# Optimization experiments

Measured on AMD Instinct MI355X. Metric: run time of the kernel, lower is better.

The kernel has to match this reference:

```python
import jax, jax.numpy as jnp
import numpy as np

N = 100000      # nodes
E = 1600000     # edges
H = 32          # hidden_channels
G = 512         # graphs in batch
F_IN = 7        # input node feature dim (fixed by GCNConv(7, H))
RRELU_SLOPE = (1.0 / 8.0 + 1.0 / 3.0) / 2.0  # eval-mode RReLU negative slope


def _rrelu(v):
    return jnp.where(v >= 0, v, RRELU_SLOPE * v)


def _gcn(x, row, col, ew, W, b):
    # GCNConv with normalize=True, add_self_loops=False
    deg = jax.ops.segment_sum(ew, col, num_segments=N)
    dis = jnp.where(deg > 0, jax.lax.rsqrt(deg), 0.0)
    norm = dis[row] * ew * dis[col]            # [E]
    h = x @ W                                  # [N, H]
    out = jax.ops.segment_sum(norm[:, None] * h[row], col, num_segments=N)
    return out + b


def setup_inputs() -> dict:
    key = jax.random.key(0)
    ks = jax.random.split(key, 12)
    s = 0.1
    x = jax.random.normal(ks[0], (N, F_IN), dtype=jnp.float32)
    edge_index = jax.random.randint(ks[1], (2, E), 0, N)
    batch = jnp.sort(jax.random.randint(ks[2], (N,), 0, G))
    edge_weights = jax.random.uniform(ks[3], (E,), dtype=jnp.float32)
    W1 = jax.random.normal(ks[4], (F_IN, H), dtype=jnp.float32) * s
    b1 = jnp.zeros((H,), jnp.float32)
    W2 = jax.random.normal(ks[5], (H, H), dtype=jnp.float32) * s
    b2 = jnp.zeros((H,), jnp.float32)
    Wl1 = jax.random.normal(ks[6], (H, H), dtype=jnp.float32) * s
    bl1 = jnp.zeros((H,), jnp.float32)
    Wl2 = jax.random.normal(ks[7], (H, H), dtype=jnp.float32) * s
    bl2 = jnp.zeros((H,), jnp.float32)
    Wl3 = jax.random.normal(ks[8], (H, 1), dtype=jnp.float32) * s
    bl3 = jnp.zeros((1,), jnp.float32)
    return dict(x=x, edge_index=edge_index, batch=batch, edge_weights=edge_weights,
                W1=W1, b1=b1, W2=W2, b2=b2, Wl1=Wl1, bl1=bl1, Wl2=Wl2, bl2=bl2,
                Wl3=Wl3, bl3=bl3)


def reference(x, edge_index, batch, edge_weights, W1, b1, W2, b2,
              Wl1, bl1, Wl2, bl2, Wl3, bl3):
    row, col = edge_index[0], edge_index[1]
    # conv1 (weighted GCN)
    x = _gcn(x, row, col, edge_weights, W1, b1)
    # max_pool_neighbor_x: max over incoming neighbors + self-loop
    self_idx = jnp.arange(N)
    x = jax.ops.segment_max(
        jnp.concatenate([x[row], x], axis=0),
        jnp.concatenate([col, self_idx], axis=0),
        num_segments=N)
    res = x
    # conv2 (unit edge weights)
    ones_ew = jnp.ones((E,), x.dtype)
    x = _gcn(x, row, col, ones_ew, W2, b2)
    x = jax.nn.relu(res + x)
    # global max pool over graphs
    x = jax.ops.segment_max(x, batch, num_segments=G)   # [G, H]
    res = x
    x = x @ Wl1 + bl1
    x = _rrelu(res + x)
    res = x
    x = x @ Wl2 + bl2
    x = _rrelu(res + x)
    # dropout: identity in eval mode
    x = x @ Wl3 + bl3
    return _rrelu(x)                                     # [G, 1]
```

## Files before the change

### kernel.cpp

```cpp
#include <hip/hip_runtime.h>
#include <hip/hip_bf16.h>

#define NN 100000
#define EE 1600000
#define HH 32
#define GG 512
#define FIN 7
#define NBUK 391
#define EPB 4096
#define P1G 391
#define BCAP 4608
#define SLOPE 0.22916666666666666f
#define QS 32767.0f
#define IQS (1.0f / 32767.0f)
#define RMASK 0x1FFFFu

typedef unsigned short bf16_t;
typedef unsigned int uint32;
typedef unsigned long long uint64;
typedef unsigned short u16v2 __attribute__((ext_vector_type(2)));

__device__ __forceinline__ bf16_t f2b(float f) {
    return (bf16_t)(__bfloat16_as_ushort(__float2bfloat16(f)));
}
__device__ __forceinline__ float b2f(bf16_t u) {
    return __uint_as_float(((uint32)u) << 16);
}
__device__ __forceinline__ float lo16(uint32 u) { return __uint_as_float(u << 16); }
__device__ __forceinline__ float hi16(uint32 u) { return __uint_as_float(u & 0xFFFF0000u); }
__device__ __forceinline__ uint32 pack2(float a, float b) {
    return (uint32)f2b(a) | ((uint32)f2b(b) << 16);
}
__device__ __forceinline__ uint32 fwd16(uint32 u) {
    return u ^ (0x80008000u | (((u >> 15) & 0x00010001u) * 0x7FFFu));
}
__device__ __forceinline__ uint32 inv16(uint32 w) {
    return w ^ (0x80008000u | ((((~w) >> 15) & 0x00010001u) * 0x7FFFu));
}
__device__ __forceinline__ uint32 pkmax(uint32 a, uint32 b) {
    u16v2 x = __builtin_bit_cast(u16v2, a);
    u16v2 y = __builtin_bit_cast(u16v2, b);
    u16v2 r = __builtin_elementwise_max(x, y);
    return __builtin_bit_cast(uint32, r);
}

__global__ __launch_bounds__(512) void k_p1(const int* __restrict__ row,
                                            const int* __restrict__ col,
                                            const float* __restrict__ ew,
                                            int* __restrict__ Pmat,
                                            uint64* __restrict__ pay) {
    __shared__ int h[512];
    __shared__ int cur[392];
    __shared__ int colc[EPB];
    int t = threadIdx.x;
    h[t] = 0;
    __syncthreads();
    int e0 = blockIdx.x * EPB, e1 = min(e0 + EPB, EE);
    int nloc = e1 - e0;
    for (int i = t; i < nloc; i += 512) {
        int c = col[e0 + i];
        colc[i] = c;
        atomicAdd(&h[c >> 8], 1);
    }
    __syncthreads();
    int c0 = h[t];
    for (int d = 1; d < 512; d <<= 1) {
        int a = (t >= d) ? h[t - d] : 0;
        __syncthreads();
        h[t] += a;
        __syncthreads();
    }
    int ex0 = h[t] - c0;
    if (t < 392) { cur[t] = ex0; Pmat[blockIdx.x * 392 + t] = ex0; }
    __syncthreads();
    uint64* bpay = pay + (size_t)blockIdx.x * EPB;
    for (int i = t; i < nloc; i += 512) {
        int c = colc[i];
        int e = e0 + i;
        uint32 q = (uint32)(ew[e] * QS + 0.5f);
        int r = atomicAdd(&cur[c >> 8], 1);
        bpay[r] = ((uint64)(uint32)(c & 255) << 32) | ((uint64)q << 17) | (uint32)row[e];
    }
}

__global__ __launch_bounds__(256) void k_p2(const int* __restrict__ Pmat,
                                            const uint64* __restrict__ pay,
                                            const float* __restrict__ x,
                                            uint32* __restrict__ spack,
                                            int* __restrict__ cnt,
                                            int* __restrict__ off,
                                            float* __restrict__ d1s,
                                            float* __restrict__ d2,
                                            uint32* __restrict__ xsu) {
    __shared__ uint64 staged[BCAP];
    __shared__ int hist[256], s[256], cur[256], qsum[256];
    __shared__ int tot;
    int b = blockIdx.x, t = threadIdx.x;
    hist[t] = 0; qsum[t] = 0;
    if (t == 0) tot = 0;
    __syncthreads();
    for (int k = t; k < P1G; k += 256) {
        int s0 = Pmat[k * 392 + b];
        int s1 = Pmat[k * 392 + b + 1];
        int len = s1 - s0;
        if (len > 0) {
            int r0 = atomicAdd(&tot, len);
            const uint64* src = pay + (size_t)k * EPB + s0;
            for (int i = 0; i < len && r0 + i < BCAP; i++) staged[r0 + i] = src[i];
        }
    }
    __syncthreads();
    int M = min(tot, BCAP);
    for (int j = t; j < M; j += 256) atomicAdd(&hist[(int)(staged[j] >> 32)], 1);
    __syncthreads();
    int v = hist[t]; s[t] = v;
    __syncthreads();
    for (int d = 1; d < 256; d <<= 1) {
        int u = (t >= d) ? s[t - d] : 0;
        __syncthreads();
        s[t] += u;
        __syncthreads();
    }
    int excl = s[t] - v;
    int gb = b * BCAP;
    int n = b * 256 + t;
    if (n < NN) { cnt[n] = v; off[n] = gb + excl; }
    cur[t] = excl;
    __syncthreads();
    for (int j = t; j < M; j += 256) {
        uint64 p = staged[j];
        int nb = (int)(p >> 32);
        int r = atomicAdd(&cur[nb], 1);
        spack[gb + r] = (uint32)p;
        atomicAdd(&qsum[nb], (int)((uint32)p >> 17));
    }
    __syncthreads();
    if (n < NN) {
        int sq = qsum[t];
        float dis1 = sq > 0 ? rsqrtf((float)sq * IQS) : 0.0f;
        d1s[n] = dis1 * IQS;
        d2[n] = v > 0 ? rsqrtf((float)v) : 0.0f;
        float f0 = x[n * FIN + 0] * dis1, f1 = x[n * FIN + 1] * dis1;
        float f2 = x[n * FIN + 2] * dis1, f3 = x[n * FIN + 3] * dis1;
        float f4 = x[n * FIN + 4] * dis1, f5 = x[n * FIN + 5] * dis1;
        float f6 = x[n * FIN + 6] * dis1;
        xsu[n * 4 + 0] = pack2(f0, f1);
        xsu[n * 4 + 1] = pack2(f2, f3);
        xsu[n * 4 + 2] = pack2(f4, f5);
        xsu[n * 4 + 3] = pack2(f6, 0.0f);
    }
}

__global__ __launch_bounds__(256) void k_agg1(const int* __restrict__ off,
                                              const int* __restrict__ cnt,
                                              const uint32* __restrict__ spack,
                                              const uint4* __restrict__ XS,
                                              const float* __restrict__ d1s,
                                              const float* __restrict__ b1,
                                              const float* __restrict__ W1,
                                              uint32* __restrict__ x1u) {
    __shared__ float sW[FIN * HH];
    int t = threadIdx.x;
    if (t < FIN * HH) sW[t] = W1[t];
    __syncthreads();
    int n = blockIdx.x * 16 + (t >> 4);
    int l = t & 15;
    int o = off[n], m = cnt[n];
    const uint32* bin = spack + o;
    float a0 = 0, a1 = 0, a2 = 0, a3 = 0, a4 = 0, a5 = 0, a6 = 0;
    for (int j = l; j < m; j += 16) {
        uint32 p = bin[j];
        uint4 v = XS[p & RMASK];
        float q = (float)(p >> 17);
        a0 += q * lo16(v.x); a1 += q * hi16(v.x);
        a2 += q * lo16(v.y); a3 += q * hi16(v.y);
        a4 += q * lo16(v.z); a5 += q * hi16(v.z);
        a6 += q * lo16(v.w);
    }
#pragma unroll
    for (int q = 8; q >= 1; q >>= 1) {
        a0 += __shfl_xor(a0, q, 16); a1 += __shfl_xor(a1, q, 16);
        a2 += __shfl_xor(a2, q, 16); a3 += __shfl_xor(a3, q, 16);
        a4 += __shfl_xor(a4, q, 16); a5 += __shfl_xor(a5, q, 16);
        a6 += __shfl_xor(a6, q, 16);
    }
    float sc = d1s[n];
    int c0 = 2 * l, c1 = 2 * l + 1;
    float s0 = a0 * sW[c0] + a1 * sW[HH + c0] + a2 * sW[2 * HH + c0]
             + a3 * sW[3 * HH + c0] + a4 * sW[4 * HH + c0]
             + a5 * sW[5 * HH + c0] + a6 * sW[6 * HH + c0];
    float s1 = a0 * sW[c1] + a1 * sW[HH + c1] + a2 * sW[2 * HH + c1]
             + a3 * sW[3 * HH + c1] + a4 * sW[4 * HH + c1]
             + a5 * sW[5 * HH + c1] + a6 * sW[6 * HH + c1];
    x1u[n * 16 + l] = fwd16(pack2(sc * s0 + b1[c0], sc * s1 + b1[c1]));
}

__global__ __launch_bounds__(256) void k_pool(const int* __restrict__ off,
                                              const int* __restrict__ cnt,
                                              const uint32* __restrict__ spack,
                                              const uint32* __restrict__ X1,
                                              const float* __restrict__ d2,
                                              uint32* __restrict__ xpu,
                                              uint32* __restrict__ xpsu) {
    int t = threadIdx.x;
    int n = blockIdx.x * 4 + (t >> 6);
    int l = t & 63;
    int eg = l >> 2, qt = l & 3;
    int o = off[n], m = cnt[n];
    const uint32* bin = spack + o;
    const uint4* X4 = (const uint4*)X1;
    uint32 binw = (l < m) ? bin[l] : 0;
    uint4 u = X4[n * 4 + qt];
    uint32 t0 = u.x, t1 = u.y, t2 = u.z, t3 = u.w;
    int mc = min(m, 64);
    for (int j0 = 0; j0 < mc; j0 += 16) {
        int j = j0 + eg;
        uint32 p = (uint32)__shfl((int)binw, j, 64);
        int r = (j < mc) ? (int)(p & RMASK) : n;
        uint4 v = X4[r * 4 + qt];
        t0 = pkmax(t0, v.x); t1 = pkmax(t1, v.y);
        t2 = pkmax(t2, v.z); t3 = pkmax(t3, v.w);
    }
    for (int j0 = 64; j0 < m; j0 += 16) {
        int j = j0 + eg;
        int r = (j < m) ? (int)(bin[j] & RMASK) : n;
        uint4 v = X4[r * 4 + qt];
        t0 = pkmax(t0, v.x); t1 = pkmax(t1, v.y);
        t2 = pkmax(t2, v.z); t3 = pkmax(t3, v.w);
    }
#pragma unroll
    for (int o2 = 4; o2 < 64; o2 <<= 1) {
        t0 = pkmax(t0, (uint32)__shfl_xor((int)t0, o2, 64));
        t1 = pkmax(t1, (uint32)__shfl_xor((int)t1, o2, 64));
        t2 = pkmax(t2, (uint32)__shfl_xor((int)t2, o2, 64));
        t3 = pkmax(t3, (uint32)__shfl_xor((int)t3, o2, 64));
    }
    if (eg == 0) {
        uint32 r0 = inv16(t0), r1 = inv16(t1), r2 = inv16(t2), r3 = inv16(t3);
        float dn = d2[n];
        uint4 w0, w1;
        w0.x = r0; w0.y = r1; w0.z = r2; w0.w = r3;
        w1.x = pack2(dn * lo16(r0), dn * hi16(r0));
        w1.y = pack2(dn * lo16(r1), dn * hi16(r1));
        w1.z = pack2(dn * lo16(r2), dn * hi16(r2));
        w1.w = pack2(dn * lo16(r3), dn * hi16(r3));
        ((uint4*)xpu)[n * 4 + qt] = w0;
        ((uint4*)xpsu)[n * 4 + qt] = w1;
    }
}

__global__ __launch_bounds__(256) void k_agg2(const int* __restrict__ off,
                                              const int* __restrict__ cnt,
                                              const uint32* __restrict__ spack,
                                              const uint32* __restrict__ XPS,
                                              float* __restrict__ Sf) {
    int t = threadIdx.x;
    int n = blockIdx.x * 4 + (t >> 6);
    int l = t & 63;
    int eg = l >> 2, qt = l & 3;
    int o = off[n], m = cnt[n];
    const uint32* bin = spack + o;
    const uint4* X4 = (const uint4*)XPS;
    uint32 binw = (l < m) ? bin[l] : 0;
    float a0 = 0, a1 = 0, a2 = 0, a3 = 0, a4 = 0, a5 = 0, a6 = 0, a7 = 0;
    int mc = min(m, 64);
    for (int j0 = 0; j0 < mc; j0 += 16) {
        int j = j0 + eg;
        uint32 p = (uint32)__shfl((int)binw, j, 64);
        if (j < mc) {
            uint4 v = X4[(p & RMASK) * 4 + qt];
            a0 += lo16(v.x); a1 += hi16(v.x);
            a2 += lo16(v.y); a3 += hi16(v.y);
            a4 += lo16(v.z); a5 += hi16(v.z);
            a6 += lo16(v.w); a7 += hi16(v.w);
        }
    }
    for (int j0 = 64; j0 < m; j0 += 16) {
        int j = j0 + eg;
        if (j < m) {
            uint4 v = X4[(bin[j] & RMASK) * 4 + qt];
            a0 += lo16(v.x); a1 += hi16(v.x);
            a2 += lo16(v.y); a3 += hi16(v.y);
            a4 += lo16(v.z); a5 += hi16(v.z);
            a6 += lo16(v.w); a7 += hi16(v.w);
        }
    }
#pragma unroll
    for (int o2 = 4; o2 < 64; o2 <<= 1) {
        a0 += __shfl_xor(a0, o2, 64); a1 += __shfl_xor(a1, o2, 64);
        a2 += __shfl_xor(a2, o2, 64); a3 += __shfl_xor(a3, o2, 64);
        a4 += __shfl_xor(a4, o2, 64); a5 += __shfl_xor(a5, o2, 64);
        a6 += __shfl_xor(a6, o2, 64); a7 += __shfl_xor(a7, o2, 64);
    }
    if (eg == 0) {
        float4 f0 = make_float4(a0, a1, a2, a3);
        float4 f1 = make_float4(a4, a5, a6, a7);
        ((float4*)Sf)[n * 8 + qt * 2] = f0;
        ((float4*)Sf)[n * 8 + qt * 2 + 1] = f1;
    }
}

__global__ __launch_bounds__(256) void k_gpool_mlp(const float* __restrict__ Sf,
                                                   const uint32* __restrict__ xpu,
                                                   const float* __restrict__ d2,
                                                   const float* __restrict__ b2,
                                                   const float* __restrict__ W2,
                                                   const int* __restrict__ batch,
                                                   const float* __restrict__ Wl1,
                                                   const float* __restrict__ bl1,
                                                   const float* __restrict__ Wl2,
                                                   const float* __restrict__ bl2,
                                                   const float* __restrict__ Wl3,
                                                   const float* __restrict__ bl3,
                                                   float* __restrict__ out) {
    __shared__ float sWc[HH * HH];
    __shared__ float sW1[HH * HH];
    __shared__ float sW2[HH * HH];
    __shared__ float sW3[HH];
    __shared__ float sred[8][HH];
    int t = threadIdx.x;
    int g = blockIdx.x;
    for (int j = t; j < HH * HH; j += 256) {
        sWc[j] = W2[j];
        sW1[j] = Wl1[j];
        sW2[j] = Wl2[j];
    }
    if (t < HH) sW3[t] = Wl3[t];
    __syncthreads();

    int lo = 0, hi = NN;
    while (lo < hi) { int mid = (lo + hi) >> 1; if (batch[mid] < g) lo = mid + 1; else hi = mid; }
    int s = lo;
    hi = NN;
    while (lo < hi) { int mid = (lo + hi) >> 1; if (batch[mid] < g + 1) lo = mid + 1; else hi = mid; }
    int e = lo;

    int c = t & 31, w = t >> 5;
    float bc = b2[c];
    float mx = -3.0e38f;
    for (int i = s + w; i < e; i += 8) {
        float sv = Sf[i * HH + c];
        float acc = 0.0f;
#pragma unroll
        for (int k = 0; k < HH; k++) acc += __shfl(sv, k, 32) * sWc[k * HH + c];
        uint32 u = xpu[i * 16 + (c >> 1)];
        float xpv = (c & 1) ? hi16(u) : lo16(u);
        float v = fmaxf(xpv + d2[i] * acc + bc, 0.0f);
        v = b2f(f2b(v));
        mx = fmaxf(mx, v);
    }
    sred[w][c] = mx;
    __syncthreads();

    if (t < HH) {
        float x0 = sred[0][t];
#pragma unroll
        for (int q = 1; q < 8; q++) x0 = fmaxf(x0, sred[q][t]);
        float acc = 0.0f;
#pragma unroll
        for (int k = 0; k < HH; k++) acc += __shfl(x0, k, 32) * sW1[k * HH + t];
        float a1 = x0 + acc + bl1[t];
        a1 = a1 >= 0.0f ? a1 : SLOPE * a1;
        float acc2 = 0.0f;
#pragma unroll
        for (int k = 0; k < HH; k++) acc2 += __shfl(a1, k, 32) * sW2[k * HH + t];
        float a2 = a1 + acc2 + bl2[t];
        a2 = a2 >= 0.0f ? a2 : SLOPE * a2;
        float p = a2 * sW3[t];
#pragma unroll
        for (int o = 16; o >= 1; o >>= 1) p += __shfl_down(p, o, 32);
        if (t == 0) {
            float o = p + bl3[0];
            o = o >= 0.0f ? o : SLOPE * o;
            out[g] = o;
        }
    }
}

extern "C" void kernel_launch(void* const* d_in, const int* in_sizes, int n_in,
                              void* d_out, int out_size, void* d_ws, size_t ws_size,
                              hipStream_t stream) {
    const float* x   = (const float*)d_in[0];
    const int*   ei  = (const int*)d_in[1];
    const int*   bat = (const int*)d_in[2];
    const float* ew  = (const float*)d_in[3];
    const float* W1  = (const float*)d_in[4];
    const float* b1  = (const float*)d_in[5];
    const float* W2  = (const float*)d_in[6];
    const float* b2  = (const float*)d_in[7];
    const float* Wl1 = (const float*)d_in[8];
    const float* bl1 = (const float*)d_in[9];
    const float* Wl2 = (const float*)d_in[10];
    const float* bl2 = (const float*)d_in[11];
    const float* Wl3 = (const float*)d_in[12];
    const float* bl3 = (const float*)d_in[13];
    float* out = (float*)d_out;

    const int* row = ei;
    const int* col = ei + EE;

    char* w = (char*)d_ws;
    uint64* pay  = (uint64*)w;  w += (size_t)P1G * EPB * 8;
    float*  Sf   = (float*)pay;
    int*   Pmat  = (int*)w;     w += (size_t)P1G * 392 * 4;
    uint32* spack = (uint32*)w; w += (size_t)NBUK * BCAP * 4;
    int*    cnt  = (int*)w;     w += NN * 4;
    int*    off  = (int*)w;     w += NN * 4;
    float*  d1s  = (float*)w;   w += NN * 4;
    float*  d2   = (float*)w;   w += NN * 4;
    uint32* xsu  = (uint32*)w;  w += (size_t)NN * 4 * 4;
    uint32* x1u  = (uint32*)w;  w += (size_t)NN * 16 * 4;
    uint32* xpu  = (uint32*)w;  w += (size_t)NN * 16 * 4;
    uint32* xpsu = (uint32*)w;  w += (size_t)NN * 16 * 4;

    k_p1   <<<P1G, 512, 0, stream>>>(row, col, ew, Pmat, pay);
    k_p2   <<<NBUK, 256, 0, stream>>>(Pmat, pay, x, spack, cnt, off, d1s, d2, xsu);
    k_agg1 <<<NN / 16, 256, 0, stream>>>(off, cnt, spack, (const uint4*)xsu, d1s, b1, W1, x1u);
    k_pool <<<NN / 4, 256, 0, stream>>>(off, cnt, spack, x1u, d2, xpu, xpsu);
    k_agg2 <<<NN / 4, 256, 0, stream>>>(off, cnt, spack, xpsu, Sf);
    k_gpool_mlp<<<GG, 256, 0, stream>>>(Sf, xpu, d2, b2, W2, bat,
                                        Wl1, bl1, Wl2, bl2, Wl3, bl3, out);
}
```

Baseline: 257.9 us.

## Split node features into two 16-channel halves for cache-resident gathers

```diff
diff --git a/kernel.cpp b/kernel.cpp
--- a/kernel.cpp
+++ b/kernel.cpp
@@ -158,7 +158,8 @@
                                               const float* __restrict__ d1s,
                                               const float* __restrict__ b1,
                                               const float* __restrict__ W1,
-                                              uint32* __restrict__ x1u) {
+                                              uint32* __restrict__ x1a,
+                                              uint32* __restrict__ x1b) {
     __shared__ float sW[FIN * HH];
     int t = threadIdx.x;
     if (t < FIN * HH) sW[t] = W1[t];
@@ -192,44 +193,46 @@
     float s1 = a0 * sW[c1] + a1 * sW[HH + c1] + a2 * sW[2 * HH + c1]
              + a3 * sW[3 * HH + c1] + a4 * sW[4 * HH + c1]
              + a5 * sW[5 * HH + c1] + a6 * sW[6 * HH + c1];
-    x1u[n * 16 + l] = fwd16(pack2(sc * s0 + b1[c0], sc * s1 + b1[c1]));
-}
-
-__global__ __launch_bounds__(256) void k_pool(const int* __restrict__ off,
-                                              const int* __restrict__ cnt,
-                                              const uint32* __restrict__ spack,
-                                              const uint32* __restrict__ X1,
-                                              const float* __restrict__ d2,
-                                              uint32* __restrict__ xpu,
-                                              uint32* __restrict__ xpsu) {
+    uint32 r = fwd16(pack2(sc * s0 + b1[c0], sc * s1 + b1[c1]));
+    if (l < 8) x1a[n * 8 + l] = r;
+    else       x1b[n * 8 + (l - 8)] = r;
+}
+
+__global__ __launch_bounds__(256) void k_poolh(const int* __restrict__ off,
+                                               const int* __restrict__ cnt,
+                                               const uint32* __restrict__ spack,
+                                               const uint32* __restrict__ X,
+                                               const float* __restrict__ d2,
+                                               uint32* __restrict__ xpO,
+                                               uint32* __restrict__ xpsO) {
     int t = threadIdx.x;
     int n = blockIdx.x * 4 + (t >> 6);
     int l = t & 63;
-    int eg = l >> 2, qt = l & 3;
+    int eg = l >> 1, qt = l & 1;
     int o = off[n], m = cnt[n];
     const uint32* bin = spack + o;
-    const uint4* X4 = (const uint4*)X1;
+    const uint4* X4 = (const uint4*)X;
     uint32 binw = (l < m) ? bin[l] : 0;
-    uint4 u = X4[n * 4 + qt];
+    uint4 u = X4[n * 2 + qt];
     uint32 t0 = u.x, t1 = u.y, t2 = u.z, t3 = u.w;
     int mc = min(m, 64);
-    for (int j0 = 0; j0 < mc; j0 += 16) {
+    for (int j0 = 0; j0 < mc; j0 += 32) {
         int j = j0 + eg;
         uint32 p = (uint32)__shfl((int)binw, j, 64);
         int r = (j < mc) ? (int)(p & RMASK) : n;
-        uint4 v = X4[r * 4 + qt];
+        uint4 v = X4[r * 2 + qt];
         t0 = pkmax(t0, v.x); t1 = pkmax(t1, v.y);
         t2 = pkmax(t2, v.z); t3 = pkmax(t3, v.w);
     }
-    for (int j0 = 64; j0 < m; j0 += 16) {
+    for (int j0 = 64; j0 < m; j0 += 32) {
         int j = j0 + eg;
         int r = (j < m) ? (int)(bin[j] & RMASK) : n;
-        uint4 v = X4[r * 4 + qt];
+        uint4 v = X4[r * 2 + qt];
         t0 = pkmax(t0, v.x); t1 = pkmax(t1, v.y);
         t2 = pkmax(t2, v.z); t3 = pkmax(t3, v.w);
     }
 #pragma unroll
-    for (int o2 = 4; o2 < 64; o2 <<= 1) {
+    for (int o2 = 2; o2 < 64; o2 <<= 1) {
         t0 = pkmax(t0, (uint32)__shfl_xor((int)t0, o2, 64));
         t1 = pkmax(t1, (uint32)__shfl_xor((int)t1, o2, 64));
         t2 = pkmax(t2, (uint32)__shfl_xor((int)t2, o2, 64));
@@ -244,41 +247,41 @@
         w1.y = pack2(dn * lo16(r1), dn * hi16(r1));
         w1.z = pack2(dn * lo16(r2), dn * hi16(r2));
         w1.w = pack2(dn * lo16(r3), dn * hi16(r3));
-        ((uint4*)xpu)[n * 4 + qt] = w0;
-        ((uint4*)xpsu)[n * 4 + qt] = w1;
-    }
-}
-
-__global__ __launch_bounds__(256) void k_agg2(const int* __restrict__ off,
+        ((uint4*)xpO)[n * 2 + qt] = w0;
+        ((uint4*)xpsO)[n * 2 + qt] = w1;
+    }
+}
+
+__global__ __launch_bounds__(256) void k_aggh(const int* __restrict__ off,
                                               const int* __restrict__ cnt,
                                               const uint32* __restrict__ spack,
                                               const uint32* __restrict__ XPS,
-                                              float* __restrict__ Sf) {
+                                              float* __restrict__ SO) {
     int t = threadIdx.x;
     int n = blockIdx.x * 4 + (t >> 6);
     int l = t & 63;
-    int eg = l >> 2, qt = l & 3;
+    int eg = l >> 1, qt = l & 1;
     int o = off[n], m = cnt[n];
     const uint32* bin = spack + o;
     const uint4* X4 = (const uint4*)XPS;
     uint32 binw = (l < m) ? bin[l] : 0;
     float a0 = 0, a1 = 0, a2 = 0, a3 = 0, a4 = 0, a5 = 0, a6 = 0, a7 = 0;
     int mc = min(m, 64);
-    for (int j0 = 0; j0 < mc; j0 += 16) {
+    for (int j0 = 0; j0 < mc; j0 += 32) {
         int j = j0 + eg;
         uint32 p = (uint32)__shfl((int)binw, j, 64);
         if (j < mc) {
-            uint4 v = X4[(p & RMASK) * 4 + qt];
+            uint4 v = X4[(p & RMASK) * 2 + qt];
             a0 += lo16(v.x); a1 += hi16(v.x);
             a2 += lo16(v.y); a3 += hi16(v.y);
             a4 += lo16(v.z); a5 += hi16(v.z);
             a6 += lo16(v.w); a7 += hi16(v.w);
         }
     }
-    for (int j0 = 64; j0 < m; j0 += 16) {
+    for (int j0 = 64; j0 < m; j0 += 32) {
         int j = j0 + eg;
         if (j < m) {
-            uint4 v = X4[(bin[j] & RMASK) * 4 + qt];
+            uint4 v = X4[(bin[j] & RMASK) * 2 + qt];
             a0 += lo16(v.x); a1 += hi16(v.x);
             a2 += lo16(v.y); a3 += hi16(v.y);
             a4 += lo16(v.z); a5 += hi16(v.z);
@@ -286,22 +289,22 @@
         }
     }
 #pragma unroll
-    for (int o2 = 4; o2 < 64; o2 <<= 1) {
+    for (int o2 = 2; o2 < 64; o2 <<= 1) {
         a0 += __shfl_xor(a0, o2, 64); a1 += __shfl_xor(a1, o2, 64);
         a2 += __shfl_xor(a2, o2, 64); a3 += __shfl_xor(a3, o2, 64);
         a4 += __shfl_xor(a4, o2, 64); a5 += __shfl_xor(a5, o2, 64);
         a6 += __shfl_xor(a6, o2, 64); a7 += __shfl_xor(a7, o2, 64);
     }
     if (eg == 0) {
-        float4 f0 = make_float4(a0, a1, a2, a3);
-        float4 f1 = make_float4(a4, a5, a6, a7);
-        ((float4*)Sf)[n * 8 + qt * 2] = f0;
-        ((float4*)Sf)[n * 8 + qt * 2 + 1] = f1;
-    }
-}
-
-__global__ __launch_bounds__(256) void k_gpool_mlp(const float* __restrict__ Sf,
-                                                   const uint32* __restrict__ xpu,
+        ((float4*)SO)[n * 4 + qt * 2]     = make_float4(a0, a1, a2, a3);
+        ((float4*)SO)[n * 4 + qt * 2 + 1] = make_float4(a4, a5, a6, a7);
+    }
+}
+
+__global__ __launch_bounds__(256) void k_gpool_mlp(const float* __restrict__ SfA,
+                                                   const float* __restrict__ SfB,
+                                                   const uint32* __restrict__ xpuA,
+                                                   const uint32* __restrict__ xpuB,
                                                    const float* __restrict__ d2,
                                                    const float* __restrict__ b2,
                                                    const float* __restrict__ W2,
@@ -339,11 +342,11 @@
     float bc = b2[c];
     float mx = -3.0e38f;
     for (int i = s + w; i < e; i += 8) {
-        float sv = Sf[i * HH + c];
+        float sv = (c < 16) ? SfA[i * 16 + c] : SfB[i * 16 + (c - 16)];
         float acc = 0.0f;
 #pragma unroll
         for (int k = 0; k < HH; k++) acc += __shfl(sv, k, 32) * sWc[k * HH + c];
-        uint32 u = xpu[i * 16 + (c >> 1)];
+        uint32 u = (c < 16 ? xpuA : xpuB)[i * 8 + ((c & 15) >> 1)];
         float xpv = (c & 1) ? hi16(u) : lo16(u);
         float v = fmaxf(xpv + d2[i] * acc + bc, 0.0f);
         v = b2f(f2b(v));
@@ -401,7 +404,8 @@
 
     char* w = (char*)d_ws;
     uint64* pay  = (uint64*)w;  w += (size_t)P1G * EPB * 8;
-    float*  Sf   = (float*)pay;
+    float*  SfA  = (float*)pay;
+    float*  SfB  = SfA + (size_t)NN * 16;
     int*   Pmat  = (int*)w;     w += (size_t)P1G * 392 * 4;
     uint32* spack = (uint32*)w; w += (size_t)NBUK * BCAP * 4;
     int*    cnt  = (int*)w;     w += NN * 4;
@@ -409,15 +413,20 @@
     float*  d1s  = (float*)w;   w += NN * 4;
     float*  d2   = (float*)w;   w += NN * 4;
     uint32* xsu  = (uint32*)w;  w += (size_t)NN * 4 * 4;
-    uint32* x1u  = (uint32*)w;  w += (size_t)NN * 16 * 4;
-    uint32* xpu  = (uint32*)w;  w += (size_t)NN * 16 * 4;
-    uint32* xpsu = (uint32*)w;  w += (size_t)NN * 16 * 4;
-
-    k_p1   <<<P1G, 512, 0, stream>>>(row, col, ew, Pmat, pay);
-    k_p2   <<<NBUK, 256, 0, stream>>>(Pmat, pay, x, spack, cnt, off, d1s, d2, xsu);
-    k_agg1 <<<NN / 16, 256, 0, stream>>>(off, cnt, spack, (const uint4*)xsu, d1s, b1, W1, x1u);
-    k_pool <<<NN / 4, 256, 0, stream>>>(off, cnt, spack, x1u, d2, xpu, xpsu);
-    k_agg2 <<<NN / 4, 256, 0, stream>>>(off, cnt, spack, xpsu, Sf);
-    k_gpool_mlp<<<GG, 256, 0, stream>>>(Sf, xpu, d2, b2, W2, bat,
+    uint32* x1a  = (uint32*)w;  w += (size_t)NN * 8 * 4;
+    uint32* x1b  = (uint32*)w;  w += (size_t)NN * 8 * 4;
+    uint32* xpuA = (uint32*)w;  w += (size_t)NN * 8 * 4;
+    uint32* xpuB = (uint32*)w;  w += (size_t)NN * 8 * 4;
+    uint32* xpsA = (uint32*)w;  w += (size_t)NN * 8 * 4;
+    uint32* xpsB = (uint32*)w;  w += (size_t)NN * 8 * 4;
+
+    k_p1    <<<P1G, 512, 0, stream>>>(row, col, ew, Pmat, pay);
+    k_p2    <<<NBUK, 256, 0, stream>>>(Pmat, pay, x, spack, cnt, off, d1s, d2, xsu);
+    k_agg1  <<<NN / 16, 256, 0, stream>>>(off, cnt, spack, (const uint4*)xsu, d1s, b1, W1, x1a, x1b);
+    k_poolh <<<NN / 4, 256, 0, stream>>>(off, cnt, spack, x1a, d2, xpuA, xpsA);
+    k_poolh <<<NN / 4, 256, 0, stream>>>(off, cnt, spack, x1b, d2, xpuB, xpsB);
+    k_aggh  <<<NN / 4, 256, 0, stream>>>(off, cnt, spack, xpsA, SfA);
+    k_aggh  <<<NN / 4, 256, 0, stream>>>(off, cnt, spack, xpsB, SfB);
+    k_gpool_mlp<<<GG, 256, 0, stream>>>(SfA, SfB, xpuA, xpuB, d2, b2, W2, bat,
                                         Wl1, bl1, Wl2, bl2, Wl3, bl3, out);
 }
```

Result: slower. 356.2 us (+38.1%).
